# Optimization experiments

Measured on AMD Instinct MI355X. Metric: run time of the kernel, lower is better.

Reference implementation:

```python
import jax, jax.numpy as jnp
import numpy as np

NUM_VOXELS = 2_000_000
NUM_CLUSTS = 2000
NUM_EDGES = 16_000
IN_FEATS = 4      # columns 1:5 of data: x, y, z, value
HIDDEN = 128
LATENT = 64       # encoder output feature size


def setup_inputs() -> dict:
    key = jax.random.key(0)
    k1, k2, k3, k4, k5, k6, k7 = jax.random.split(key, 7)
    data = jax.random.normal(k1, (NUM_VOXELS, 5), dtype=jnp.float32)
    clust_ids = jax.random.randint(k2, (NUM_VOXELS,), 0, NUM_CLUSTS)
    edge_index = jax.random.randint(k3, (2, NUM_EDGES), 0, NUM_CLUSTS)
    # encoder (pool + MLP) parameters
    W1 = jax.random.normal(k4, (IN_FEATS, HIDDEN), dtype=jnp.float32) / np.sqrt(IN_FEATS)
    b1 = jnp.zeros((HIDDEN,), dtype=jnp.float32)
    W2 = jax.random.normal(k5, (HIDDEN, LATENT), dtype=jnp.float32) / np.sqrt(HIDDEN)
    b2 = jnp.zeros((LATENT,), dtype=jnp.float32)
    return {"data": data, "clust_ids": clust_ids, "edge_index": edge_index,
            "W1": W1, "b1": b1, "W2": W2, "b2": b2}


def reference(data, clust_ids, edge_index, W1, b1, W2, b2):
    # Vectorized replacement of the per-edge python loop:
    # the loop builds, per edge i, the union of voxels of clusters (e0, e1)
    # with batch column overwritten by i; the encoder then globally pools
    # per edge-id. Equivalent: per-cluster sums via one segment_sum pass,
    # then per-edge mean over the union of the two clusters.
    feat = data[:, 1:5]                                   # [N, 4]
    clust_sum = jax.ops.segment_sum(feat, clust_ids, num_segments=NUM_CLUSTS)  # [C, 4]
    clust_cnt = jax.ops.segment_sum(jnp.ones((data.shape[0],), dtype=feat.dtype),
                                    clust_ids, num_segments=NUM_CLUSTS)        # [C]
    e0, e1 = edge_index[0], edge_index[1]
    pooled = (clust_sum[e0] + clust_sum[e1]) / jnp.maximum(clust_cnt[e0] + clust_cnt[e1], 1.0)[:, None]  # [E, 4]
    h = jax.nn.relu(pooled @ W1 + b1)                     # [E, HIDDEN]
    feats = h @ W2 + b2                                   # [E, LATENT]
    return feats
```

## Files before the change

kernel.cpp:

```cpp
#include <hip/hip_runtime.h>

#define NUM_VOXELS 2000000
#define NUM_CLUSTS 2000
#define NUM_EDGES  16000

#define ST   2048
#define ACCN (5 * ST)

#define FSCALE  65536.0f
#define FINV    (1.0f / 65536.0f)
#define BIASF   8.0f
#define BIAS_FS (8.0f * 65536.0f)

#define A_BLOCKS  512
#define A_THREADS 1024
#define RED_CH    64
#define NCH       (A_BLOCKS / RED_CH)

typedef float  f4v __attribute__((ext_vector_type(4)));
typedef int    i4v __attribute__((ext_vector_type(4)));
typedef unsigned long long u64;

__device__ __forceinline__ u64 pack2(float a, float b) {
    unsigned lo = (unsigned)__float2int_rn(fmaf(a, FSCALE, BIAS_FS));
    unsigned hi = (unsigned)__float2int_rn(fmaf(b, FSCALE, BIAS_FS));
    return (u64)lo | ((u64)hi << 32);
}

__global__ __launch_bounds__(A_THREADS) void seg_accum(
        const float* __restrict__ data,
        const int* __restrict__ cids,
        int* __restrict__ part) {
    __shared__ __align__(16) int ls[ACCN];
    u64* s01 = (u64*)ls;
    u64* s23 = (u64*)(ls + 4096);
    int* scnt = ls + 8192;
    for (int o = threadIdx.x; o < ACCN; o += A_THREADS) ls[o] = 0;
    __syncthreads();

    const int ngroups = NUM_VOXELS / 4;
    for (int g = blockIdx.x * A_THREADS + threadIdx.x; g < ngroups;
         g += gridDim.x * A_THREADS) {
        const f4v* dp = (const f4v*)(data + 20ull * (unsigned)g);
        f4v q0 = __builtin_nontemporal_load(dp + 0);
        f4v q1 = __builtin_nontemporal_load(dp + 1);
        f4v q2 = __builtin_nontemporal_load(dp + 2);
        f4v q3 = __builtin_nontemporal_load(dp + 3);
        f4v q4 = __builtin_nontemporal_load(dp + 4);
        i4v c4 = __builtin_nontemporal_load((const i4v*)(cids + 4ull * (unsigned)g));

        atomicAdd(&s01[c4.x], pack2(q0.y, q0.z));
        atomicAdd(&s23[c4.x], pack2(q0.w, q1.x));
        atomicAdd(&scnt[c4.x], 1);
        atomicAdd(&s01[c4.y], pack2(q1.z, q1.w));
        atomicAdd(&s23[c4.y], pack2(q2.x, q2.y));
        atomicAdd(&scnt[c4.y], 1);
        atomicAdd(&s01[c4.z], pack2(q2.w, q3.x));
        atomicAdd(&s23[c4.z], pack2(q3.y, q3.z));
        atomicAdd(&scnt[c4.z], 1);
        atomicAdd(&s01[c4.w], pack2(q4.x, q4.y));
        atomicAdd(&s23[c4.w], pack2(q4.z, q4.w));
        atomicAdd(&scnt[c4.w], 1);
    }
    __syncthreads();

    int* p = part + (size_t)blockIdx.x * ACCN;
    for (int o = threadIdx.x; o < ACCN; o += A_THREADS) p[o] = ls[o];
}

__global__ __launch_bounds__(A_THREADS) void seg_accum_atomic(
        const float* __restrict__ data,
        const int* __restrict__ cids,
        int* __restrict__ acc) {
    __shared__ __align__(16) int ls[ACCN];
    u64* s01 = (u64*)ls;
    u64* s23 = (u64*)(ls + 4096);
    int* scnt = ls + 8192;
    for (int o = threadIdx.x; o < ACCN; o += A_THREADS) ls[o] = 0;
    __syncthreads();
    const int ngroups = NUM_VOXELS / 4;
    for (int g = blockIdx.x * A_THREADS + threadIdx.x; g < ngroups;
         g += gridDim.x * A_THREADS) {
        const f4v* dp = (const f4v*)(data + 20ull * (unsigned)g);
        f4v q0 = dp[0], q1 = dp[1], q2 = dp[2], q3 = dp[3], q4 = dp[4];
        i4v c4 = *(const i4v*)(cids + 4ull * (unsigned)g);
        atomicAdd(&s01[c4.x], pack2(q0.y, q0.z));
        atomicAdd(&s23[c4.x], pack2(q0.w, q1.x));
        atomicAdd(&scnt[c4.x], 1);
        atomicAdd(&s01[c4.y], pack2(q1.z, q1.w));
        atomicAdd(&s23[c4.y], pack2(q2.x, q2.y));
        atomicAdd(&scnt[c4.y], 1);
        atomicAdd(&s01[c4.z], pack2(q2.w, q3.x));
        atomicAdd(&s23[c4.z], pack2(q3.y, q3.z));
        atomicAdd(&scnt[c4.z], 1);
        atomicAdd(&s01[c4.w], pack2(q4.x, q4.y));
        atomicAdd(&s23[c4.w], pack2(q4.z, q4.w));
        atomicAdd(&scnt[c4.w], 1);
    }
    __syncthreads();
    for (int o = threadIdx.x; o < ACCN; o += A_THREADS) {
        int v = ls[o];
        if (v != 0) atomicAdd(&acc[o], v);
    }
}

__global__ __launch_bounds__(256) void seg_reduce(
        const int* __restrict__ part, int* __restrict__ part2) {
    const int i = blockIdx.x * 256 + threadIdx.x;
    const int* p = part + (size_t)blockIdx.y * RED_CH * ACCN + i;
    int s0 = 0, s1 = 0, s2 = 0, s3 = 0;
#pragma unroll
    for (int b = 0; b < RED_CH; b += 4) {
        s0 += p[(size_t)(b + 0) * ACCN];
        s1 += p[(size_t)(b + 1) * ACCN];
        s2 += p[(size_t)(b + 2) * ACCN];
        s3 += p[(size_t)(b + 3) * ACCN];
    }
    part2[(size_t)blockIdx.y * ACCN + i] = (s0 + s1) + (s2 + s3);
}

__global__ __launch_bounds__(256) void clust_final(
        const int* __restrict__ part2, float* __restrict__ clustf, int nch) {
    const int c = blockIdx.x * 256 + threadIdx.x;
    if (c >= NUM_CLUSTS) return;
    int s0 = 0, s1 = 0, s2 = 0, s3 = 0, cn = 0;
    for (int ch = 0; ch < nch; ++ch) {
        const int* p = part2 + (size_t)ch * ACCN;
        s0 += p[2 * c];
        s1 += p[2 * c + 1];
        s2 += p[4096 + 2 * c];
        s3 += p[4096 + 2 * c + 1];
        cn += p[8192 + c];
    }
    const float fc = (float)cn;
    float4 v;
    v.x = fmaf((float)s0, FINV, -BIASF * fc);
    v.y = fmaf((float)s1, FINV, -BIASF * fc);
    v.z = fmaf((float)s2, FINV, -BIASF * fc);
    v.w = fmaf((float)s3, FINV, -BIASF * fc);
    *(float4*)&clustf[c * 8] = v;
    clustf[c * 8 + 4] = fc;
}

#define E_BLOCKS 500
#define E_THREADS 256
#define EPW 8

__global__ __launch_bounds__(E_THREADS) void edge_mlp(
        const float* __restrict__ clustf,
        const int* __restrict__ eidx,
        const float* __restrict__ W1, const float* __restrict__ b1,
        const float* __restrict__ W2, const float* __restrict__ b2,
        float* __restrict__ out) {
    __shared__ float hbuf[E_THREADS / 64][2][128];
    const int lane = threadIdx.x & 63;
    const int w = threadIdx.x >> 6;
    const int wg = blockIdx.x * (E_THREADS / 64) + w;
    const int ebase = wg * EPW;

    float w1a[4], w1b[4];
#pragma unroll
    for (int c = 0; c < 4; ++c) {
        w1a[c] = W1[c * 128 + lane];
        w1b[c] = W1[c * 128 + 64 + lane];
    }
    const float b1a = b1[lane];
    const float b1b = b1[64 + lane];
    const float b2j = b2[lane];
    float w2c[128];
#pragma unroll
    for (int k = 0; k < 128; ++k) w2c[k] = W2[k * 64 + lane];

    int ids0[EPW], ids1[EPW];
    {
        i4v a = *(const i4v*)&eidx[ebase];
        i4v b = *(const i4v*)&eidx[ebase + 4];
        ids0[0] = a.x; ids0[1] = a.y; ids0[2] = a.z; ids0[3] = a.w;
        ids0[4] = b.x; ids0[5] = b.y; ids0[6] = b.z; ids0[7] = b.w;
        i4v c = *(const i4v*)&eidx[NUM_EDGES + ebase];
        i4v d = *(const i4v*)&eidx[NUM_EDGES + ebase + 4];
        ids1[0] = c.x; ids1[1] = c.y; ids1[2] = c.z; ids1[3] = c.w;
        ids1[4] = d.x; ids1[5] = d.y; ids1[6] = d.z; ids1[7] = d.w;
    }

#pragma unroll
    for (int i = 0; i < EPW; ++i) {
        const int e0 = ids0[i], e1 = ids1[i];
        const float4 sa = *(const float4*)&clustf[e0 * 8];
        const float  ca = clustf[e0 * 8 + 4];
        const float4 sb = *(const float4*)&clustf[e1 * 8];
        const float  cb = clustf[e1 * 8 + 4];
        const float rden = 1.0f / fmaxf(ca + cb, 1.0f);
        const float p0 = (sa.x + sb.x) * rden;
        const float p1 = (sa.y + sb.y) * rden;
        const float p2 = (sa.z + sb.z) * rden;
        const float p3 = (sa.w + sb.w) * rden;

        float ha = b1a + p0 * w1a[0] + p1 * w1a[1] + p2 * w1a[2] + p3 * w1a[3];
        float hb = b1b + p0 * w1b[0] + p1 * w1b[1] + p2 * w1b[2] + p3 * w1b[3];
        ha = fmaxf(ha, 0.0f);
        hb = fmaxf(hb, 0.0f);

        float* hx = hbuf[w][i & 1];
        hx[lane] = ha;
        hx[64 + lane] = hb;

        float a0 = b2j, a1 = 0.f, a2 = 0.f, a3 = 0.f;
#pragma unroll
        for (int k = 0; k < 128; k += 16) {
            float4 h4;
            h4 = *(const float4*)&hx[k];
            a0 += h4.x * w2c[k] + h4.y * w2c[k + 1] + h4.z * w2c[k + 2] + h4.w * w2c[k + 3];
            h4 = *(const float4*)&hx[k + 4];
            a1 += h4.x * w2c[k + 4] + h4.y * w2c[k + 5] + h4.z * w2c[k + 6] + h4.w * w2c[k + 7];
            h4 = *(const float4*)&hx[k + 8];
            a2 += h4.x * w2c[k + 8] + h4.y * w2c[k + 9] + h4.z * w2c[k + 10] + h4.w * w2c[k + 11];
            h4 = *(const float4*)&hx[k + 12];
            a3 += h4.x * w2c[k + 12] + h4.y * w2c[k + 13] + h4.z * w2c[k + 14] + h4.w * w2c[k + 15];
        }
        out[(size_t)(ebase + i) * 64 + lane] = (a0 + a1) + (a2 + a3);
    }
}

extern "C" void kernel_launch(void* const* d_in, const int* in_sizes, int n_in,
                              void* d_out, int out_size, void* d_ws, size_t ws_size,
                              hipStream_t stream) {
    const float* data = (const float*)d_in[0];
    const int* cids   = (const int*)d_in[1];
    const int* eidx   = (const int*)d_in[2];
    const float* W1   = (const float*)d_in[3];
    const float* b1   = (const float*)d_in[4];
    const float* W2   = (const float*)d_in[5];
    const float* b2   = (const float*)d_in[6];
    float* out = (float*)d_out;
    int* ws = (int*)d_ws;

    const size_t full_need =
        ((size_t)A_BLOCKS + NCH) * ACCN * sizeof(int) + NUM_CLUSTS * 8 * sizeof(float);
    if (ws_size >= full_need) {
        int* part  = ws;
        int* part2 = ws + (size_t)A_BLOCKS * ACCN;
        float* clustf = (float*)(ws + (size_t)(A_BLOCKS + NCH) * ACCN);
        seg_accum<<<A_BLOCKS, A_THREADS, 0, stream>>>(data, cids, part);
        seg_reduce<<<dim3(ACCN / 256, NCH), 256, 0, stream>>>(part, part2);
        clust_final<<<(NUM_CLUSTS + 255) / 256, 256, 0, stream>>>(part2, clustf, NCH);
        edge_mlp<<<E_BLOCKS, E_THREADS, 0, stream>>>(clustf, eidx, W1, b1, W2, b2, out);
    } else {
        int* img = ws;
        float* clustf = (float*)(ws + ACCN);
        hipMemsetAsync(img, 0, ACCN * sizeof(int), stream);
        seg_accum_atomic<<<A_BLOCKS, A_THREADS, 0, stream>>>(data, cids, img);
        clust_final<<<(NUM_CLUSTS + 255) / 256, 256, 0, stream>>>(img, clustf, 1);
        edge_mlp<<<E_BLOCKS, E_THREADS, 0, stream>>>(clustf, eidx, W1, b1, W2, b2, out);
    }
}
```

Baseline: 125.8 us.

## Merge reduction stages into atomic in-place combine and fold decode into edge MLP

Halves the number of accumulation blocks and swaps nontemporal loads for ordinary loads. The two-stage reduce plus cluster-finalise kernels become a single kernel that sums chunks of partials and atomically adds them into block 0's image in place. The fixed-point decode (scale and bias removal) moves into the edge MLP, which now reads the integer image directly. This cuts two kernel launches and intermediate buffers, at the cost of global atomics and fewer accumulation blocks (less parallelism for the main streaming pass).

```diff
diff --git a/kernel.cpp b/kernel.cpp
--- a/kernel.cpp
+++ b/kernel.cpp
@@ -12,7 +12,7 @@
 #define BIASF   8.0f
 #define BIAS_FS (8.0f * 65536.0f)
 
-#define A_BLOCKS  512
+#define A_BLOCKS  256
 #define A_THREADS 1024
 #define RED_CH    64
 #define NCH       (A_BLOCKS / RED_CH)
@@ -42,12 +42,12 @@
     for (int g = blockIdx.x * A_THREADS + threadIdx.x; g < ngroups;
          g += gridDim.x * A_THREADS) {
         const f4v* dp = (const f4v*)(data + 20ull * (unsigned)g);
-        f4v q0 = __builtin_nontemporal_load(dp + 0);
-        f4v q1 = __builtin_nontemporal_load(dp + 1);
-        f4v q2 = __builtin_nontemporal_load(dp + 2);
-        f4v q3 = __builtin_nontemporal_load(dp + 3);
-        f4v q4 = __builtin_nontemporal_load(dp + 4);
-        i4v c4 = __builtin_nontemporal_load((const i4v*)(cids + 4ull * (unsigned)g));
+        f4v q0 = dp[0];
+        f4v q1 = dp[1];
+        f4v q2 = dp[2];
+        f4v q3 = dp[3];
+        f4v q4 = dp[4];
+        i4v c4 = *(const i4v*)(cids + 4ull * (unsigned)g);
 
         atomicAdd(&s01[c4.x], pack2(q0.y, q0.z));
         atomicAdd(&s23[c4.x], pack2(q0.w, q1.x));
@@ -104,42 +104,13 @@
     }
 }
 
-__global__ __launch_bounds__(256) void seg_reduce(
-        const int* __restrict__ part, int* __restrict__ part2) {
+__global__ __launch_bounds__(256) void seg_combine(int* __restrict__ part) {
     const int i = blockIdx.x * 256 + threadIdx.x;
-    const int* p = part + (size_t)blockIdx.y * RED_CH * ACCN + i;
-    int s0 = 0, s1 = 0, s2 = 0, s3 = 0;
-#pragma unroll
-    for (int b = 0; b < RED_CH; b += 4) {
-        s0 += p[(size_t)(b + 0) * ACCN];
-        s1 += p[(size_t)(b + 1) * ACCN];
-        s2 += p[(size_t)(b + 2) * ACCN];
-        s3 += p[(size_t)(b + 3) * ACCN];
-    }
-    part2[(size_t)blockIdx.y * ACCN + i] = (s0 + s1) + (s2 + s3);
-}
-
-__global__ __launch_bounds__(256) void clust_final(
-        const int* __restrict__ part2, float* __restrict__ clustf, int nch) {
-    const int c = blockIdx.x * 256 + threadIdx.x;
-    if (c >= NUM_CLUSTS) return;
-    int s0 = 0, s1 = 0, s2 = 0, s3 = 0, cn = 0;
-    for (int ch = 0; ch < nch; ++ch) {
-        const int* p = part2 + (size_t)ch * ACCN;
-        s0 += p[2 * c];
-        s1 += p[2 * c + 1];
-        s2 += p[4096 + 2 * c];
-        s3 += p[4096 + 2 * c + 1];
-        cn += p[8192 + c];
-    }
-    const float fc = (float)cn;
-    float4 v;
-    v.x = fmaf((float)s0, FINV, -BIASF * fc);
-    v.y = fmaf((float)s1, FINV, -BIASF * fc);
-    v.z = fmaf((float)s2, FINV, -BIASF * fc);
-    v.w = fmaf((float)s3, FINV, -BIASF * fc);
-    *(float4*)&clustf[c * 8] = v;
-    clustf[c * 8 + 4] = fc;
+    const int b0 = blockIdx.y * RED_CH + (blockIdx.y == 0 ? 1 : 0);
+    const int b1 = blockIdx.y * RED_CH + RED_CH;
+    int s = 0;
+    for (int b = b0; b < b1; ++b) s += part[(size_t)b * ACCN + i];
+    atomicAdd(&part[i], s);
 }
 
 #define E_BLOCKS 500
@@ -147,7 +118,7 @@
 #define EPW 8
 
 __global__ __launch_bounds__(E_THREADS) void edge_mlp(
-        const float* __restrict__ clustf,
+        const int* __restrict__ img,
         const int* __restrict__ eidx,
         const float* __restrict__ W1, const float* __restrict__ b1,
         const float* __restrict__ W2, const float* __restrict__ b2,
@@ -186,15 +157,17 @@
 #pragma unroll
     for (int i = 0; i < EPW; ++i) {
         const int e0 = ids0[i], e1 = ids1[i];
-        const float4 sa = *(const float4*)&clustf[e0 * 8];
-        const float  ca = clustf[e0 * 8 + 4];
-        const float4 sb = *(const float4*)&clustf[e1 * 8];
-        const float  cb = clustf[e1 * 8 + 4];
-        const float rden = 1.0f / fmaxf(ca + cb, 1.0f);
-        const float p0 = (sa.x + sb.x) * rden;
-        const float p1 = (sa.y + sb.y) * rden;
-        const float p2 = (sa.z + sb.z) * rden;
-        const float p3 = (sa.w + sb.w) * rden;
+        const i4v fa = {img[2 * e0], img[2 * e0 + 1],
+                        img[4096 + 2 * e0], img[4096 + 2 * e0 + 1]};
+        const i4v fb = {img[2 * e1], img[2 * e1 + 1],
+                        img[4096 + 2 * e1], img[4096 + 2 * e1 + 1]};
+        const float cnt = (float)img[8192 + e0] + (float)img[8192 + e1];
+        const float rden = 1.0f / fmaxf(cnt, 1.0f);
+        const float bt = -BIASF * cnt;
+        const float p0 = fmaf((float)fa.x + (float)fb.x, FINV, bt) * rden;
+        const float p1 = fmaf((float)fa.y + (float)fb.y, FINV, bt) * rden;
+        const float p2 = fmaf((float)fa.z + (float)fb.z, FINV, bt) * rden;
+        const float p3 = fmaf((float)fa.w + (float)fb.w, FINV, bt) * rden;
 
         float ha = b1a + p0 * w1a[0] + p1 * w1a[1] + p2 * w1a[2] + p3 * w1a[3];
         float hb = b1b + p0 * w1b[0] + p1 * w1b[1] + p2 * w1b[2] + p3 * w1b[3];
@@ -235,22 +208,15 @@
     float* out = (float*)d_out;
     int* ws = (int*)d_ws;
 
-    const size_t full_need =
-        ((size_t)A_BLOCKS + NCH) * ACCN * sizeof(int) + NUM_CLUSTS * 8 * sizeof(float);
-    if (ws_size >= full_need) {
-        int* part  = ws;
-        int* part2 = ws + (size_t)A_BLOCKS * ACCN;
-        float* clustf = (float*)(ws + (size_t)(A_BLOCKS + NCH) * ACCN);
+    if (ws_size >= (size_t)A_BLOCKS * ACCN * sizeof(int)) {
+        int* part = ws;
         seg_accum<<<A_BLOCKS, A_THREADS, 0, stream>>>(data, cids, part);
-        seg_reduce<<<dim3(ACCN / 256, NCH), 256, 0, stream>>>(part, part2);
-        clust_final<<<(NUM_CLUSTS + 255) / 256, 256, 0, stream>>>(part2, clustf, NCH);
-        edge_mlp<<<E_BLOCKS, E_THREADS, 0, stream>>>(clustf, eidx, W1, b1, W2, b2, out);
+        seg_combine<<<dim3(ACCN / 256, NCH), 256, 0, stream>>>(part);
+        edge_mlp<<<E_BLOCKS, E_THREADS, 0, stream>>>(part, eidx, W1, b1, W2, b2, out);
     } else {
         int* img = ws;
-        float* clustf = (float*)(ws + ACCN);
         hipMemsetAsync(img, 0, ACCN * sizeof(int), stream);
         seg_accum_atomic<<<A_BLOCKS, A_THREADS, 0, stream>>>(data, cids, img);
-        clust_final<<<(NUM_CLUSTS + 255) / 256, 256, 0, stream>>>(img, clustf, 1);
-        edge_mlp<<<E_BLOCKS, E_THREADS, 0, stream>>>(clustf, eidx, W1, b1, W2, b2, out);
-    }
-}
+        edge_mlp<<<E_BLOCKS, E_THREADS, 0, stream>>>(img, eidx, W1, b1, W2, b2, out);
+    }
+}
```

New measurement: 117.9 us. 6.2% less time.
